# Kernel tuning notes

Measured on AMD Instinct MI355X. Metric: run time of the kernel, lower is better.

## Reference

```python
import jax, jax.numpy as jnp
import numpy as np

EPS = 1e-5

def _bn(x, g, b):
    # training-mode BatchNorm1d over the batch axis (axis 0), biased variance
    m = jnp.mean(x, axis=0)
    v = jnp.var(x, axis=0)
    return g * (x - m) / jnp.sqrt(v + EPS) + b

def _mlp(x, w1, b1, g1, be1, w2, b2, g2, be2, w3, b3):
    # Linear -> BN -> ReLU -> Linear -> BN -> ReLU -> Linear
    x = jax.nn.relu(_bn(x @ w1.T + b1, g1, be1))
    x = jax.nn.relu(_bn(x @ w2.T + b2, g2, be2))
    return x @ w3.T + b3

def setup_inputs() -> dict:
    key = jax.random.key(0)
    ks = jax.random.split(key, 10)
    B, S, D = 256, 512, 128
    w = lambda k: jax.random.normal(k, (D, D), jnp.float32) * 0.05
    return {
        "s": jax.random.normal(ks[0], (B, S, D), jnp.float32),
        "c": jax.random.normal(ks[1], (B, D), jnp.float32),
        "s_w1": w(ks[2]), "s_b1": jnp.zeros((D,), jnp.float32),
        "s_g1": jnp.ones((D,), jnp.float32), "s_be1": jnp.zeros((D,), jnp.float32),
        "s_w2": w(ks[3]), "s_b2": jnp.zeros((D,), jnp.float32),
        "s_g2": jnp.ones((D,), jnp.float32), "s_be2": jnp.zeros((D,), jnp.float32),
        "s_w3": w(ks[4]), "s_b3": jnp.zeros((D,), jnp.float32),
        "c_w1": w(ks[5]), "c_b1": jnp.zeros((D,), jnp.float32),
        "c_g1": jnp.ones((D,), jnp.float32), "c_be1": jnp.zeros((D,), jnp.float32),
        "c_w2": w(ks[6]), "c_b2": jnp.zeros((D,), jnp.float32),
        "c_g2": jnp.ones((D,), jnp.float32), "c_be2": jnp.zeros((D,), jnp.float32),
        "c_w3": w(ks[7]), "c_b3": jnp.zeros((D,), jnp.float32),
    }

def reference(s, c,
              s_w1, s_b1, s_g1, s_be1, s_w2, s_b2, s_g2, s_be2, s_w3, s_b3,
              c_w1, c_b1, c_g1, c_be1, c_w2, c_b2, c_g2, c_be2, c_w3, c_b3):
    # c_mlp: [B, D] -> [B, D] (BN over batch)
    c_out = _mlp(c, c_w1, c_b1, c_g1, c_be1, c_w2, c_b2, c_g2, c_be2, c_w3, c_b3)
    # s_mlp applied per sequence slice; BN stats over batch axis 0 only
    # (matches the torch loop where each s[:, i, :] gets its own BN stats).
    # s: [B, S, D]; _bn with axis=0 gives per-(slice, feature) stats.
    s_h = _mlp(s, s_w1, s_b1, s_g1, s_be1, s_w2, s_b2, s_g2, s_be2, s_w3, s_b3)
    s_out = s_h * c_out[:, None, :]          # context gate, [B, S, D]
    aggregated_c = jnp.max(s_out, axis=1)    # pooling == 'max', [B, D]
    return (s_out, aggregated_c)
```

## Files before the change

### kernel.cpp

```cpp
#include <hip/hip_runtime.h>
#include <hip/hip_bf16.h>
#include <math.h>

#define BATCH 256
#define SEQ   512
#define DIM   128
#define LDSK  136
#define LDSF  132

typedef __attribute__((ext_vector_type(8))) __bf16  bf16x8;
typedef __attribute__((ext_vector_type(4))) __bf16  bf16x4;
typedef __attribute__((ext_vector_type(4))) float   f32x4;

template<int RT, bool WF32>
__device__ __forceinline__ void matmul_layer(
    const __bf16* __restrict__ Xa, const void* __restrict__ wg,
    const float* bias, f32x4 (&acc)[RT][8], int wave, int m, int q)
{
  const __bf16* wgh = (const __bf16*)wg;
  const float*  wgf = (const float*)wg;
  const int rowbase = wave * RT * 16;
#pragma unroll
  for (int ct = 0; ct < 8; ++ct) {
    const float b = bias[ct * 16 + m];
    const f32x4 bv = {b, b, b, b};
#pragma unroll
    for (int rt = 0; rt < RT; ++rt) acc[rt][ct] = bv;
  }
#pragma unroll
  for (int ks = 0; ks < 4; ++ks) {
    const int k0 = ks * 32 + q * 8;
    bf16x8 a[RT], bw[8];
#pragma unroll
    for (int rt = 0; rt < RT; ++rt)
      a[rt] = *(const bf16x8*)(Xa + (rowbase + rt * 16 + m) * LDSK + k0);
#pragma unroll
    for (int ct = 0; ct < 8; ++ct) {
      if constexpr (WF32) {
        const float4 u0 = *(const float4*)(wgf + (ct * 16 + m) * DIM + k0);
        const float4 u1 = *(const float4*)(wgf + (ct * 16 + m) * DIM + k0 + 4);
        bw[ct] = (bf16x8){(__bf16)u0.x, (__bf16)u0.y, (__bf16)u0.z, (__bf16)u0.w,
                          (__bf16)u1.x, (__bf16)u1.y, (__bf16)u1.z, (__bf16)u1.w};
      } else {
        bw[ct] = *(const bf16x8*)(wgh + (ct * 16 + m) * DIM + k0);
      }
    }
#pragma unroll
    for (int rt = 0; rt < RT; ++rt)
#pragma unroll
      for (int ct = 0; ct < 8; ++ct)
        acc[rt][ct] = __builtin_amdgcn_mfma_f32_16x16x32_bf16(a[rt], bw[ct], acc[rt][ct], 0, 0, 0);
  }
}

template<int RT>
__device__ __forceinline__ void stats_accum(
    const f32x4 (&acc)[RT][8], float* sumL, float* sqL, int m, int q)
{
#pragma unroll
  for (int ct = 0; ct < 8; ++ct) {
    float s = 0.f, ss = 0.f;
#pragma unroll
    for (int rt = 0; rt < RT; ++rt)
#pragma unroll
      for (int r = 0; r < 4; ++r) { const float v = acc[rt][ct][r]; s += v; ss += v * v; }
    s  += __shfl_xor(s, 16, 64);  s  += __shfl_xor(s, 32, 64);
    ss += __shfl_xor(ss, 16, 64); ss += __shfl_xor(ss, 32, 64);
    if (q == 0) { atomicAdd(&sumL[ct * 16 + m], s); atomicAdd(&sqL[ct * 16 + m], ss); }
  }
}

template<int RT>
__device__ __forceinline__ void bn_relu_store(
    const f32x4 (&acc)[RT][8], __bf16* Xa, const float* sumL, const float* sqL,
    const float* g, const float* be, int wave, int m, int q)
{
  const int rowbase = wave * RT * 16;
#pragma unroll
  for (int ct = 0; ct < 8; ++ct) {
    const int n = ct * 16 + m;
    const float mean = sumL[n] * (1.0f / BATCH);
    const float var  = sqL[n]  * (1.0f / BATCH) - mean * mean;
    const float a = g[n] * rsqrtf(var + 1e-5f);
    const float c = be[n] - a * mean;
#pragma unroll
    for (int rt = 0; rt < RT; ++rt)
#pragma unroll
      for (int r = 0; r < 4; ++r) {
        const float y = fmaxf(0.f, a * acc[rt][ct][r] + c);
        const int row = rowbase + rt * 16 + q * 4 + r;
        Xa[row * LDSK + n] = (__bf16)y;
      }
  }
}

template<int NW, bool GATE, bool WF32>
__device__ __forceinline__ void mlp_body(
    const float* __restrict__ x0, long xstride, int slice,
    const void* __restrict__ w1, const void* __restrict__ w2, const void* __restrict__ w3,
    const float* __restrict__ b1, const float* __restrict__ g1, const float* __restrict__ be1,
    const float* __restrict__ b2, const float* __restrict__ g2, const float* __restrict__ be2,
    const float* __restrict__ b3,
    const float* __restrict__ gate, float* __restrict__ out)
{
  static_assert(NW == 4, "epilogue assumes NW=4/RT=4");
  const int tid  = threadIdx.x;
  constexpr int NT = NW * 64;
  constexpr int RT = 16 / NW;
  const int wave = tid >> 6, lane = tid & 63;
  const int m = lane & 15, q = lane >> 4;

  __shared__ __align__(16) char XaRaw[BATCH * LDSK * 2];
  __bf16* Xa = (__bf16*)XaRaw;
  __shared__ float sum1[DIM], sq1[DIM], sum2[DIM], sq2[DIM];
  __shared__ float prm[7 * DIM];

  for (int t = tid; t < DIM; t += NT) { sum1[t] = 0.f; sq1[t] = 0.f; sum2[t] = 0.f; sq2[t] = 0.f; }
  if (tid < DIM) {
    prm[tid]           = b1[tid];  prm[DIM + tid]     = g1[tid];  prm[2 * DIM + tid] = be1[tid];
    prm[3 * DIM + tid] = b2[tid];  prm[4 * DIM + tid] = g2[tid];  prm[5 * DIM + tid] = be2[tid];
    prm[6 * DIM + tid] = b3[tid];
  }

  {
    const int rpi = NT / 32;
    const int r0  = tid >> 5;
    const int c4  = (tid & 31) * 4;
#pragma unroll
    for (int it = 0; it < BATCH / rpi; ++it) {
      const int r = it * rpi + r0;
      const float4 v = *(const float4*)(x0 + (long)r * xstride + c4);
      bf16x4 h = { (__bf16)v.x, (__bf16)v.y, (__bf16)v.z, (__bf16)v.w };
      *(bf16x4*)(Xa + r * LDSK + c4) = h;
    }
  }
  __syncthreads();

  f32x4 acc[RT][8];

  matmul_layer<RT, WF32>(Xa, w1, prm, acc, wave, m, q);
  stats_accum<RT>(acc, sum1, sq1, m, q);
  __syncthreads();
  bn_relu_store<RT>(acc, Xa, sum1, sq1, prm + DIM, prm + 2 * DIM, wave, m, q);

  matmul_layer<RT, WF32>(Xa, w2, prm + 3 * DIM, acc, wave, m, q);
  stats_accum<RT>(acc, sum2, sq2, m, q);
  __syncthreads();
  bn_relu_store<RT>(acc, Xa, sum2, sq2, prm + 4 * DIM, prm + 5 * DIM, wave, m, q);

  matmul_layer<RT, WF32>(Xa, w3, prm + 6 * DIM, acc, wave, m, q);

  if constexpr (GATE) {
    float* Xf = (float*)XaRaw;
    const int c4l = (tid & 31) * 4;
    const int r0  = tid >> 5;
    __syncthreads();
#pragma unroll
    for (int rt = 0; rt < RT; ++rt) {
      float* buf = Xf + (rt & 1) * 64 * LDSF;
#pragma unroll
      for (int ct = 0; ct < 8; ++ct)
#pragma unroll
        for (int r = 0; r < 4; ++r)
          buf[(wave * 16 + q * 4 + r) * LDSF + ct * 16 + m] = acc[rt][ct][r];
      __syncthreads();
#pragma unroll
      for (int it = 0; it < 8; ++it) {
        const int crow = it * 8 + r0;
        const int grow = (crow >> 4) * 64 + rt * 16 + (crow & 15);
        float4 y = *(const float4*)(buf + crow * LDSF + c4l);
        const float4 gv = *(const float4*)(gate + grow * DIM + c4l);
        y.x *= gv.x; y.y *= gv.y; y.z *= gv.z; y.w *= gv.w;
        *(float4*)(out + ((long)grow * SEQ + slice) * DIM + c4l) = y;
      }
    }
  } else {
    const int rowbase = wave * RT * 16;
#pragma unroll
    for (int ct = 0; ct < 8; ++ct) {
      const int col = ct * 16 + m;
#pragma unroll
      for (int rt = 0; rt < RT; ++rt) {
#pragma unroll
        for (int r = 0; r < 4; ++r) {
          const int row = rowbase + rt * 16 + q * 4 + r;
          out[row * DIM + col] = acc[rt][ct][r];
        }
      }
    }
  }
}

__global__ __launch_bounds__(256, 2)
void prep_c_kernel(const float* __restrict__ s_w1, const float* __restrict__ s_w2,
                   const float* __restrict__ s_w3, __bf16* __restrict__ wbf,
                   const float* __restrict__ c,
                   const float* __restrict__ c_w1, const float* __restrict__ c_w2,
                   const float* __restrict__ c_w3,
                   const float* __restrict__ c_b1, const float* __restrict__ c_g1,
                   const float* __restrict__ c_be1,
                   const float* __restrict__ c_b2, const float* __restrict__ c_g2,
                   const float* __restrict__ c_be2,
                   const float* __restrict__ c_b3,
                   float* __restrict__ c_out)
{
  if (blockIdx.x < 48) {
    const int idx = blockIdx.x * 256 + threadIdx.x;
    const int mi  = idx >> 12;
    const int j   = (idx & 4095) * 4;
    const float* srcs[3] = {s_w1, s_w2, s_w3};
    const float4 v = *(const float4*)(srcs[mi] + j);
    bf16x4 h = { (__bf16)v.x, (__bf16)v.y, (__bf16)v.z, (__bf16)v.w };
    *(bf16x4*)(wbf + mi * 16384 + j) = h;
    return;
  }
  mlp_body<4, false, true>(c, (long)DIM, 0,
                           c_w1, c_w2, c_w3,
                           c_b1, c_g1, c_be1, c_b2, c_g2, c_be2, c_b3,
                           nullptr, c_out);
}

__global__ __launch_bounds__(256, 2)
void s_mlp_kernel(const float* __restrict__ s, const __bf16* __restrict__ wbf,
                  const float* __restrict__ s_b1, const float* __restrict__ s_g1,
                  const float* __restrict__ s_be1,
                  const float* __restrict__ s_b2, const float* __restrict__ s_g2,
                  const float* __restrict__ s_be2,
                  const float* __restrict__ s_b3,
                  const float* __restrict__ c_out, float* __restrict__ out)
{
  mlp_body<4, true, false>(s + (long)blockIdx.x * DIM, (long)SEQ * DIM, blockIdx.x,
                           wbf, wbf + 16384, wbf + 2 * 16384,
                           s_b1, s_g1, s_be1, s_b2, s_g2, s_be2, s_b3,
                           c_out, out);
}

__global__ __launch_bounds__(1024) void maxpool_kernel(
    const float* __restrict__ sout, float* __restrict__ agg)
{
  __shared__ float4 red[1024];
  const int b = blockIdx.x;
  const int t = threadIdx.x;
  const int c4 = (t & 31) * 4, rg = t >> 5;
  const float* p = sout + (long)b * SEQ * DIM + c4;
  float4 mx = {-INFINITY, -INFINITY, -INFINITY, -INFINITY};
#pragma unroll 4
  for (int i = rg; i < SEQ; i += 32) {
    const float4 v = *(const float4*)(p + (long)i * DIM);
    mx.x = fmaxf(mx.x, v.x); mx.y = fmaxf(mx.y, v.y);
    mx.z = fmaxf(mx.z, v.z); mx.w = fmaxf(mx.w, v.w);
  }
  red[t] = mx;
  __syncthreads();
  if (t < 32) {
    float4 a = red[t];
#pragma unroll
    for (int k = 1; k < 32; ++k) {
      const float4 v = red[t + 32 * k];
      a.x = fmaxf(a.x, v.x); a.y = fmaxf(a.y, v.y);
      a.z = fmaxf(a.z, v.z); a.w = fmaxf(a.w, v.w);
    }
    *(float4*)(agg + b * DIM + c4) = a;
  }
}

extern "C" void kernel_launch(void* const* d_in, const int* in_sizes, int n_in,
                              void* d_out, int out_size, void* d_ws, size_t ws_size,
                              hipStream_t stream)
{
  const float* s     = (const float*)d_in[0];
  const float* c     = (const float*)d_in[1];
  const float* s_w1  = (const float*)d_in[2];
  const float* s_b1  = (const float*)d_in[3];
  const float* s_g1  = (const float*)d_in[4];
  const float* s_be1 = (const float*)d_in[5];
  const float* s_w2  = (const float*)d_in[6];
  const float* s_b2  = (const float*)d_in[7];
  const float* s_g2  = (const float*)d_in[8];
  const float* s_be2 = (const float*)d_in[9];
  const float* s_w3  = (const float*)d_in[10];
  const float* s_b3  = (const float*)d_in[11];
  const float* c_w1  = (const float*)d_in[12];
  const float* c_b1  = (const float*)d_in[13];
  const float* c_g1  = (const float*)d_in[14];
  const float* c_be1 = (const float*)d_in[15];
  const float* c_w2  = (const float*)d_in[16];
  const float* c_b2  = (const float*)d_in[17];
  const float* c_g2  = (const float*)d_in[18];
  const float* c_be2 = (const float*)d_in[19];
  const float* c_w3  = (const float*)d_in[20];
  const float* c_b3  = (const float*)d_in[21];

  float* out   = (float*)d_out;
  float* c_out = (float*)d_ws;
  __bf16* wbf  = (__bf16*)((char*)d_ws + (size_t)BATCH * DIM * sizeof(float));

  prep_c_kernel<<<49, 256, 0, stream>>>(
      s_w1, s_w2, s_w3, wbf,
      c, c_w1, c_w2, c_w3,
      c_b1, c_g1, c_be1, c_b2, c_g2, c_be2, c_b3, c_out);

  s_mlp_kernel<<<SEQ, 256, 0, stream>>>(
      s, wbf,
      s_b1, s_g1, s_be1, s_b2, s_g2, s_be2, s_b3,
      c_out, out);

  maxpool_kernel<<<BATCH, 1024, 0, stream>>>(out, out + (long)BATCH * SEQ * DIM);
}
```

Baseline: 240.1 us.

## Load first-layer MLP inputs directly from global memory, widen c-MLP block to 8 waves

The first matmul layer now reads the fp32 input rows straight from global memory into registers and converts them to bf16 there, instead of staging the whole 256x128 slice through LDS first. This removes the cooperative staging loop and its LDS writes. The c-MLP prep kernel moves to 512-thread blocks with 8 waves (RT=2), using half as many blocks for the weight conversion. The catch is uncoalesced, strided global reads of the s tensor: each lane fetches 32 bytes from rows spaced SEQ*DIM apart.

```diff
diff --git a/kernel.cpp b/kernel.cpp
--- a/kernel.cpp
+++ b/kernel.cpp
@@ -13,8 +13,8 @@
 typedef __attribute__((ext_vector_type(4))) float   f32x4;
 
 template<int RT, bool WF32>
-__device__ __forceinline__ void matmul_layer(
-    const __bf16* __restrict__ Xa, const void* __restrict__ wg,
+__device__ __forceinline__ void matmul_layer1(
+    const float* __restrict__ x0, long xstride, const void* __restrict__ wg,
     const float* bias, f32x4 (&acc)[RT][8], int wave, int m, int q)
 {
   const __bf16* wgh = (const __bf16*)wg;
@@ -32,8 +32,13 @@
     const int k0 = ks * 32 + q * 8;
     bf16x8 a[RT], bw[8];
 #pragma unroll
-    for (int rt = 0; rt < RT; ++rt)
-      a[rt] = *(const bf16x8*)(Xa + (rowbase + rt * 16 + m) * LDSK + k0);
+    for (int rt = 0; rt < RT; ++rt) {
+      const float* src = x0 + (long)(rowbase + rt * 16 + m) * xstride + k0;
+      const float4 u0 = *(const float4*)(src);
+      const float4 u1 = *(const float4*)(src + 4);
+      a[rt] = (bf16x8){(__bf16)u0.x, (__bf16)u0.y, (__bf16)u0.z, (__bf16)u0.w,
+                       (__bf16)u1.x, (__bf16)u1.y, (__bf16)u1.z, (__bf16)u1.w};
+    }
 #pragma unroll
     for (int ct = 0; ct < 8; ++ct) {
       if constexpr (WF32) {
@@ -53,6 +58,47 @@
   }
 }
 
+template<int RT, bool WF32>
+__device__ __forceinline__ void matmul_layer(
+    const __bf16* __restrict__ Xa, const void* __restrict__ wg,
+    const float* bias, f32x4 (&acc)[RT][8], int wave, int m, int q)
+{
+  const __bf16* wgh = (const __bf16*)wg;
+  const float*  wgf = (const float*)wg;
+  const int rowbase = wave * RT * 16;
+#pragma unroll
+  for (int ct = 0; ct < 8; ++ct) {
+    const float b = bias[ct * 16 + m];
+    const f32x4 bv = {b, b, b, b};
+#pragma unroll
+    for (int rt = 0; rt < RT; ++rt) acc[rt][ct] = bv;
+  }
+#pragma unroll
+  for (int ks = 0; ks < 4; ++ks) {
+    const int k0 = ks * 32 + q * 8;
+    bf16x8 a[RT], bw[8];
+#pragma unroll
+    for (int rt = 0; rt < RT; ++rt)
+      a[rt] = *(const bf16x8*)(Xa + (rowbase + rt * 16 + m) * LDSK + k0);
+#pragma unroll
+    for (int ct = 0; ct < 8; ++ct) {
+      if constexpr (WF32) {
+        const float4 u0 = *(const float4*)(wgf + (ct * 16 + m) * DIM + k0);
+        const float4 u1 = *(const float4*)(wgf + (ct * 16 + m) * DIM + k0 + 4);
+        bw[ct] = (bf16x8){(__bf16)u0.x, (__bf16)u0.y, (__bf16)u0.z, (__bf16)u0.w,
+                          (__bf16)u1.x, (__bf16)u1.y, (__bf16)u1.z, (__bf16)u1.w};
+      } else {
+        bw[ct] = *(const bf16x8*)(wgh + (ct * 16 + m) * DIM + k0);
+      }
+    }
+#pragma unroll
+    for (int rt = 0; rt < RT; ++rt)
+#pragma unroll
+      for (int ct = 0; ct < 8; ++ct)
+        acc[rt][ct] = __builtin_amdgcn_mfma_f32_16x16x32_bf16(a[rt], bw[ct], acc[rt][ct], 0, 0, 0);
+  }
+}
+
 template<int RT>
 __device__ __forceinline__ void stats_accum(
     const f32x4 (&acc)[RT][8], float* sumL, float* sqL, int m, int q)
@@ -103,7 +149,7 @@
     const float* __restrict__ b3,
     const float* __restrict__ gate, float* __restrict__ out)
 {
-  static_assert(NW == 4, "epilogue assumes NW=4/RT=4");
+  static_assert(!GATE || NW == 4, "gate epilogue assumes NW=4/RT=4");
   const int tid  = threadIdx.x;
   constexpr int NT = NW * 64;
   constexpr int RT = 16 / NW;
@@ -121,24 +167,11 @@
     prm[3 * DIM + tid] = b2[tid];  prm[4 * DIM + tid] = g2[tid];  prm[5 * DIM + tid] = be2[tid];
     prm[6 * DIM + tid] = b3[tid];
   }
-
-  {
-    const int rpi = NT / 32;
-    const int r0  = tid >> 5;
-    const int c4  = (tid & 31) * 4;
-#pragma unroll
-    for (int it = 0; it < BATCH / rpi; ++it) {
-      const int r = it * rpi + r0;
-      const float4 v = *(const float4*)(x0 + (long)r * xstride + c4);
-      bf16x4 h = { (__bf16)v.x, (__bf16)v.y, (__bf16)v.z, (__bf16)v.w };
-      *(bf16x4*)(Xa + r * LDSK + c4) = h;
-    }
-  }
   __syncthreads();
 
   f32x4 acc[RT][8];
 
-  matmul_layer<RT, WF32>(Xa, w1, prm, acc, wave, m, q);
+  matmul_layer1<RT, WF32>(x0, xstride, w1, prm, acc, wave, m, q);
   stats_accum<RT>(acc, sum1, sq1, m, q);
   __syncthreads();
   bn_relu_store<RT>(acc, Xa, sum1, sq1, prm + DIM, prm + 2 * DIM, wave, m, q);
@@ -191,7 +224,7 @@
   }
 }
 
-__global__ __launch_bounds__(256, 2)
+__global__ __launch_bounds__(512, 1)
 void prep_c_kernel(const float* __restrict__ s_w1, const float* __restrict__ s_w2,
                    const float* __restrict__ s_w3, __bf16* __restrict__ wbf,
                    const float* __restrict__ c,
@@ -204,8 +237,8 @@
                    const float* __restrict__ c_b3,
                    float* __restrict__ c_out)
 {
-  if (blockIdx.x < 48) {
-    const int idx = blockIdx.x * 256 + threadIdx.x;
+  if (blockIdx.x < 24) {
+    const int idx = blockIdx.x * 512 + threadIdx.x;
     const int mi  = idx >> 12;
     const int j   = (idx & 4095) * 4;
     const float* srcs[3] = {s_w1, s_w2, s_w3};
@@ -214,7 +247,7 @@
     *(bf16x4*)(wbf + mi * 16384 + j) = h;
     return;
   }
-  mlp_body<4, false, true>(c, (long)DIM, 0,
+  mlp_body<8, false, true>(c, (long)DIM, 0,
                            c_w1, c_w2, c_w3,
                            c_b1, c_g1, c_be1, c_b2, c_g2, c_be2, c_b3,
                            nullptr, c_out);
@@ -295,7 +328,7 @@
   float* c_out = (float*)d_ws;
   __bf16* wbf  = (__bf16*)((char*)d_ws + (size_t)BATCH * DIM * sizeof(float));
 
-  prep_c_kernel<<<49, 256, 0, stream>>>(
+  prep_c_kernel<<<25, 512, 0, stream>>>(
       s_w1, s_w2, s_w3, wbf,
       c, c_w1, c_w2, c_w3,
       c_b1, c_g1, c_be1, c_b2, c_g2, c_be2, c_b3, c_out);
```

Result: slower. 253.6 us (+5.6%).
